# Kernel tuning notes

Measured on AMD Instinct MI355X. Metric: run time of the kernel, lower is better.

The kernel has to match this reference:

```python
import jax, jax.numpy as jnp
import numpy as np

DIM = 512
NUM_HEADS = 16
RANK = 4
HEAD_DIM = DIM // NUM_HEADS
SCALE = HEAD_DIM ** -0.5
B_, N, NW = 2048, 49, 64


def setup_inputs() -> dict:
    key = jax.random.key(0)
    ks = jax.random.split(key, 9)
    x = jax.random.normal(ks[0], (B_, N, DIM), dtype=jnp.float32)
    mask = jax.random.normal(ks[1], (NW, N, N), dtype=jnp.float32)
    # qkv base linear (torch Linear stores weight [out,in])
    W_qkv = jax.random.normal(ks[2], (3 * DIM, DIM), dtype=jnp.float32) * (DIM ** -0.5)
    b_qkv = jax.random.normal(ks[3], (3 * DIM,), dtype=jnp.float32) * 0.02
    # LoRA down [rank, dim], up [3*dim, rank] (zero-init in module; use small random for non-trivial math)
    A_down = jax.random.normal(ks[4], (RANK, DIM), dtype=jnp.float32) * 0.02
    B_up = jax.random.normal(ks[5], (3 * DIM, RANK), dtype=jnp.float32) * 0.02
    W_proj = jax.random.normal(ks[6], (DIM, DIM), dtype=jnp.float32) * (DIM ** -0.5)
    b_proj = jax.random.normal(ks[7], (DIM,), dtype=jnp.float32) * 0.02
    return {"x": x, "mask": mask, "W_qkv": W_qkv, "b_qkv": b_qkv,
            "A_down": A_down, "B_up": B_up, "W_proj": W_proj, "b_proj": b_proj}


def reference(x, mask, W_qkv, b_qkv, A_down, B_up, W_proj, b_proj):
    Bw, n, C = x.shape
    H, hd = NUM_HEADS, HEAD_DIM
    # LoRA-augmented QKV projection: base linear + up(down(x))
    qkv = x @ W_qkv.T + b_qkv + (x @ A_down.T) @ B_up.T          # [B_, N, 3C]
    qkv = qkv.reshape(Bw, n, 3, H, hd)
    q = qkv[:, :, 0].transpose(0, 2, 1, 3)                        # [B_, H, N, hd]
    k = qkv[:, :, 1].transpose(0, 2, 1, 3)
    v = qkv[:, :, 2].transpose(0, 2, 1, 3)
    attn = jnp.einsum('bhnd,bhmd->bhnm', q, k) * SCALE            # [B_, H, N, N]
    nW = mask.shape[0]
    attn = attn.reshape(Bw // nW, nW, H, n, n) + mask[None, :, None]
    attn = attn.reshape(Bw, H, n, n)
    attn = jax.nn.softmax(attn, axis=-1)
    out = jnp.einsum('bhnm,bhmd->bhnd', attn, v)                  # [B_, H, N, hd]
    out = out.transpose(0, 2, 1, 3).reshape(Bw, n, C)
    return out @ W_proj.T + b_proj
```

## Files before the change

### kernel.cpp

```cpp
#include <hip/hip_runtime.h>
#include <stdint.h>

typedef __attribute__((ext_vector_type(4))) float f32x4;
typedef __attribute__((ext_vector_type(8))) __bf16 bf16x8;
typedef __attribute__((ext_vector_type(4))) unsigned int u32x4;
typedef __attribute__((ext_vector_type(4))) unsigned short u16x4;

#define TOK 49
#define NHEAD 16
#define HDIM 32
#define CDIM 512
#define NB 2048
#define MTOT (NB * TOK)
#define ATT_SCALE 0.17677669529663687f

__device__ __forceinline__ unsigned short f2bf(float f) {
  uint32_t u = __builtin_bit_cast(uint32_t, f);
  u += 0x7FFFu + ((u >> 16) & 1u);
  return (unsigned short)(u >> 16);
}

__device__ __forceinline__ void gl_lds16(const void* g, const void* lds) {
  __builtin_amdgcn_global_load_lds(
      (__attribute__((address_space(1))) void*)(uintptr_t)g,
      (__attribute__((address_space(3))) void*)(uint32_t)(uintptr_t)lds,
      16, 0, 0);
}

__device__ __forceinline__ f32x4 mfma16(bf16x8 a, bf16x8 b, f32x4 c) {
  return __builtin_amdgcn_mfma_f32_16x16x32_bf16(a, b, c, 0, 0, 0);
}

__global__ __launch_bounds__(256) void k_prep_weff(
    const float* __restrict__ Wqkv, const float* __restrict__ Bup,
    const float* __restrict__ Adown, unsigned short* __restrict__ weff) {
  int idx = blockIdx.x * 256 + threadIdx.x;
  if (idx >= 3 * CDIM * CDIM) return;
  int o = idx >> 9, i = idx & 511;
  float v = Wqkv[idx];
#pragma unroll
  for (int r = 0; r < 4; r++) v += Bup[o * 4 + r] * Adown[r * 512 + i];
  weff[idx] = f2bf(v);
}

__global__ __launch_bounds__(256) void k_conv4(
    const float* __restrict__ src, unsigned short* __restrict__ dst, int n4) {
  for (int i = blockIdx.x * blockDim.x + threadIdx.x; i < n4;
       i += gridDim.x * blockDim.x) {
    f32x4 v = *(const f32x4*)(src + (size_t)i * 4);
    u16x4 o;
    o[0] = f2bf(v[0]); o[1] = f2bf(v[1]); o[2] = f2bf(v[2]); o[3] = f2bf(v[3]);
    *(u16x4*)(dst + (size_t)i * 4) = o;
  }
}

template <int NT, bool SPLIT>
__global__ __launch_bounds__(512, 1) void k_gemm256(
    const unsigned short* __restrict__ A, const unsigned short* __restrict__ Bw,
    const float* __restrict__ bias,
    unsigned short* __restrict__ qo, unsigned short* __restrict__ ko,
    unsigned short* __restrict__ vo, float* __restrict__ fo) {
  __shared__ __attribute__((aligned(16))) unsigned short smem[65536];
  const int t = threadIdx.x;
  const int l = t & 63;
  const int l15 = l & 15, lq = l >> 4;
  const int w = t >> 6;
  const int wr = w >> 2, wc = w & 3;
  const int bid = blockIdx.x;
  const int lb = (bid & 7) * ((int)gridDim.x >> 3) + (bid >> 3);
  const int mt = lb / NT, nt = lb % NT;
  const size_t m0 = (size_t)mt * 256;
  const int n0 = nt * 256;

  auto stageA = [&](int kt, int bb) {
    unsigned short* dst = smem + bb * 16384;
#pragma unroll
    for (int q = 0; q < 4; ++q) {
      const int li = q * 512 + t;
      const int row = li >> 3, sl = li & 7;
      gl_lds16(A + (m0 + row) * CDIM + kt * 64 + ((sl ^ (row & 7)) << 3),
               &dst[li * 8]);
    }
  };
  auto stageB = [&](int kt, int bb) {
    unsigned short* dst = smem + 32768 + bb * 16384;
#pragma unroll
    for (int q = 0; q < 4; ++q) {
      const int li = q * 512 + t;
      const int row = li >> 3, sl = li & 7;
      gl_lds16(Bw + (size_t)(n0 + row) * CDIM + kt * 64 + ((sl ^ (row & 7)) << 3),
               &dst[li * 8]);
    }
  };

  f32x4 acc[8][4] = {};
  stageA(0, 0);
  stageB(0, 0);
  for (int kt = 0; kt < 8; ++kt) {
    const int cur = kt & 1;
    if (kt < 7) {
      stageA(kt + 1, cur ^ 1);
      stageB(kt + 1, cur ^ 1);
      asm volatile("s_waitcnt vmcnt(8)" ::: "memory");
    } else {
      asm volatile("s_waitcnt vmcnt(0)" ::: "memory");
    }
    __builtin_amdgcn_s_barrier();
    asm volatile("" ::: "memory");
    const unsigned short* bufA = smem + cur * 16384;
    const unsigned short* bufB = smem + 32768 + cur * 16384;

    bf16x8 bfr[4][2];
#pragma unroll
    for (int c = 0; c < 4; ++c) {
      const int r = wc * 64 + c * 16 + l15;
#pragma unroll
      for (int h = 0; h < 2; ++h)
        bfr[c][h] = __builtin_bit_cast(
            bf16x8,
            *(const u32x4*)&bufB[r * 64 + (((lq + h * 4) ^ (r & 7)) << 3)]);
    }

    auto loadA = [&](bf16x8(&dst)[2][2], int p) {
#pragma unroll
      for (int rr = 0; rr < 2; ++rr) {
        const int r = wr * 128 + (p * 2 + rr) * 16 + l15;
#pragma unroll
        for (int h = 0; h < 2; ++h)
          dst[rr][h] = __builtin_bit_cast(
              bf16x8,
              *(const u32x4*)&bufA[r * 64 + (((lq + h * 4) ^ (r & 7)) << 3)]);
      }
    };

    bf16x8 afA[2][2], afB[2][2];
    loadA(afA, 0);
#pragma unroll
    for (int p = 0; p < 4; ++p) {
      bf16x8(&cur_)[2][2] = (p & 1) ? afB : afA;
      bf16x8(&nxt_)[2][2] = (p & 1) ? afA : afB;
      if (p < 3) loadA(nxt_, p + 1);
      __builtin_amdgcn_s_setprio(1);
#pragma unroll
      for (int rr = 0; rr < 2; ++rr) {
#pragma unroll
        for (int c = 0; c < 4; ++c) {
          acc[p * 2 + rr][c] = mfma16(cur_[rr][0], bfr[c][0], acc[p * 2 + rr][c]);
          acc[p * 2 + rr][c] = mfma16(cur_[rr][1], bfr[c][1], acc[p * 2 + rr][c]);
        }
      }
      __builtin_amdgcn_s_setprio(0);
    }
    asm volatile("" ::: "memory");
    __builtin_amdgcn_s_barrier();
  }

  __syncthreads();
  if constexpr (SPLIT) {
    unsigned short* ep = smem + w * 8192;
#pragma unroll
    for (int J = 0; J < 4; ++J) {
      const int colb = n0 + wc * 64 + J * 16 + l15;
      const float bv = bias[colb];
#pragma unroll
      for (int I = 0; I < 8; ++I) {
#pragma unroll
        for (int r = 0; r < 4; ++r)
          ep[(I * 16 + lq * 4 + r) * 64 + J * 16 + l15] =
              f2bf(acc[I][J][r] + bv);
      }
    }
    __syncthreads();
#pragma unroll
    for (int rnd = 0; rnd < 16; ++rnd) {
      const int sub = rnd * 16 + (l >> 2);
      const int mloc = sub >> 1, hd2 = sub & 1;
      const int colh = n0 + wc * 64 + hd2 * 32;
      const int which = colh >> 9;
      const int hh = (colh >> 5) & 15;
      unsigned short* dst = which == 0 ? qo : (which == 1 ? ko : vo);
      const uint32_t mg = (uint32_t)(m0 + wr * 128 + mloc);
      const uint32_t bw_ = mg / 49u;
      const uint32_t nn = mg - bw_ * 49u;
      u32x4 v = *(const u32x4*)&ep[mloc * 64 + hd2 * 32 + (l & 3) * 8];
      *(u32x4*)&dst[((size_t)(bw_ * 16u + hh) * 49u + nn) * 32u + (l & 3) * 8] =
          v;
    }
  } else {
    float* ep32 = (float*)smem + w * 4096;
#pragma unroll
    for (int ch = 0; ch < 2; ++ch) {
#pragma unroll
      for (int J = 0; J < 4; ++J) {
        const int colb = n0 + wc * 64 + J * 16 + l15;
        const float bv = bias[colb];
#pragma unroll
        for (int Ii = 0; Ii < 4; ++Ii) {
#pragma unroll
          for (int r = 0; r < 4; ++r)
            ep32[(Ii * 16 + lq * 4 + r) * 64 + J * 16 + l15] =
                acc[ch * 4 + Ii][J][r] + bv;
        }
      }
      __syncthreads();
#pragma unroll
      for (int rnd = 0; rnd < 16; ++rnd) {
        const int row = rnd * 4 + (l >> 4);
        f32x4 v = *(const f32x4*)&ep32[row * 64 + (l & 15) * 4];
        const size_t mg = m0 + wr * 128 + ch * 64 + row;
        *(f32x4*)&fo[mg * CDIM + n0 + wc * 64 + (l & 15) * 4] = v;
      }
      __syncthreads();
    }
  }
}

__global__ __launch_bounds__(256) void k_attn(
    const unsigned short* __restrict__ qb, const unsigned short* __restrict__ kb,
    const unsigned short* __restrict__ vb, const float* __restrict__ mask,
    unsigned short* __restrict__ ao) {
  __shared__ __attribute__((aligned(16))) unsigned short sP[4][64 * 64];
  __shared__ __attribute__((aligned(16))) unsigned short sV[4][32 * 64];
  const int t = threadIdx.x;
  const int l = t & 63, w = t >> 6;
  const int l15 = l & 15, lq = l >> 4;
  const int pair = blockIdx.x * 4 + w;
  const int b = pair >> 4, h = pair & 15;
  const size_t base = (size_t)pair * (TOK * HDIM);
  unsigned short* P = sP[w];
  unsigned short* Vt = sV[w];

  bf16x8 qf[4], kf[4];
#pragma unroll
  for (int i = 0; i < 4; i++)
    qf[i] = __builtin_bit_cast(
        bf16x8, *(const u32x4*)(qb + base + (size_t)(i * 16 + l15) * 32 + lq * 8));
#pragma unroll
  for (int i = 0; i < 4; i++)
    kf[i] = __builtin_bit_cast(
        bf16x8, *(const u32x4*)(kb + base + (size_t)(i * 16 + l15) * 32 + lq * 8));
  u32x4 vr[4];
#pragma unroll
  for (int j = 0; j < 4; j++)
    vr[j] = *(const u32x4*)(vb + base + (size_t)l * 32 + j * 8);

  f32x4 s[4][4];
  __builtin_amdgcn_s_setprio(1);
#pragma unroll
  for (int i = 0; i < 4; i++) {
#pragma unroll
    for (int j = 0; j < 4; j++) s[i][j] = mfma16(qf[i], kf[j], (f32x4)0.0f);
  }
  __builtin_amdgcn_s_setprio(0);

  const bool vok = (l < TOK);
  const int tsl = ((l >> 3) & 7);
  const int tlo = l & 7;
#pragma unroll
  for (int j = 0; j < 4; j++) {
#pragma unroll
    for (int c = 0; c < 4; c++) {
      uint32_t u = vr[j][c];
      int d0 = j * 8 + c * 2;
      Vt[(d0 + 0) * 64 + ((tsl ^ ((d0 + 0) & 7)) << 3) + tlo] =
          vok ? (unsigned short)(u & 0xFFFFu) : (unsigned short)0;
      Vt[(d0 + 1) * 64 + ((tsl ^ ((d0 + 1) & 7)) << 3) + tlo] =
          vok ? (unsigned short)(u >> 16) : (unsigned short)0;
    }
  }

  const float* mrow = mask + (size_t)(b & 63) * (TOK * TOK);
#pragma unroll
  for (int i = 0; i < 4; i++) {
#pragma unroll
    for (int r = 0; r < 4; r++) {
      int row = i * 16 + lq * 4 + r;
#pragma unroll
      for (int j = 0; j < 4; j++) {
        int col = j * 16 + l15;
        float xv = s[i][j][r] * ATT_SCALE;
        if (col < TOK) {
          if (row < TOK) xv += mrow[row * TOK + col];
        } else {
          xv = -1e30f;
        }
        s[i][j][r] = xv;
      }
    }
  }

  float rinv[4][4];
#pragma unroll
  for (int i = 0; i < 4; i++) {
#pragma unroll
    for (int r = 0; r < 4; r++) {
      float m = fmaxf(fmaxf(s[i][0][r], s[i][1][r]), fmaxf(s[i][2][r], s[i][3][r]));
      m = fmaxf(m, __shfl_xor(m, 1));
      m = fmaxf(m, __shfl_xor(m, 2));
      m = fmaxf(m, __shfl_xor(m, 4));
      m = fmaxf(m, __shfl_xor(m, 8));
      float sum = 0.f;
      int row = i * 16 + lq * 4 + r;
#pragma unroll
      for (int j = 0; j < 4; j++) {
        float p = __expf(s[i][j][r] - m);
        sum += p;
        P[row * 64 + (((j * 2 + (l15 >> 3)) ^ (row & 7)) << 3) + (l15 & 7)] =
            f2bf(p);
      }
      sum += __shfl_xor(sum, 1);
      sum += __shfl_xor(sum, 2);
      sum += __shfl_xor(sum, 4);
      sum += __shfl_xor(sum, 8);
      rinv[i][r] = 1.0f / sum;
    }
  }

  asm volatile("s_waitcnt lgkmcnt(0)" ::: "memory");
  __builtin_amdgcn_sched_barrier(0);

  f32x4 o[4][2] = {};
#pragma unroll
  for (int ks = 0; ks < 2; ks++) {
    bf16x8 pa[4], vf[2];
#pragma unroll
    for (int i = 0; i < 4; i++)
      pa[i] = __builtin_bit_cast(
          bf16x8,
          *(const u32x4*)&P[(i * 16 + l15) * 64 + (((lq + ks * 4) ^ (l15 & 7)) << 3)]);
#pragma unroll
    for (int j = 0; j < 2; j++)
      vf[j] = __builtin_bit_cast(
          bf16x8,
          *(const u32x4*)&Vt[(j * 16 + l15) * 64 + (((lq + ks * 4) ^ (l15 & 7)) << 3)]);
    __builtin_amdgcn_s_setprio(1);
#pragma unroll
    for (int i = 0; i < 4; i++) {
#pragma unroll
      for (int j = 0; j < 2; j++) o[i][j] = mfma16(pa[i], vf[j], o[i][j]);
    }
    __builtin_amdgcn_s_setprio(0);
  }

#pragma unroll
  for (int i = 0; i < 4; i++) {
#pragma unroll
    for (int r = 0; r < 4; r++) {
      int row = i * 16 + lq * 4 + r;
      if (row < TOK) {
        float inv = rinv[i][r];
        size_t obase = ((size_t)b * TOK + row) * CDIM + h * HDIM;
#pragma unroll
        for (int j = 0; j < 2; j++)
          ao[obase + j * 16 + l15] = f2bf(o[i][j][r] * inv);
      }
    }
  }
}

extern "C" void kernel_launch(void* const* d_in, const int* in_sizes, int n_in,
                              void* d_out, int out_size, void* d_ws,
                              size_t ws_size, hipStream_t stream) {
  const float* x = (const float*)d_in[0];
  const float* mask = (const float*)d_in[1];
  const float* Wqkv = (const float*)d_in[2];
  const float* bqkv = (const float*)d_in[3];
  const float* Adown = (const float*)d_in[4];
  const float* Bup = (const float*)d_in[5];
  const float* Wproj = (const float*)d_in[6];
  const float* bproj = (const float*)d_in[7];
  float* out = (float*)d_out;
  char* ws = (char*)d_ws;

  size_t off = 0;
  auto alloc = [&](size_t bytes) {
    size_t o = off;
    off += (bytes + 255) & ~(size_t)255;
    return o;
  };
  const size_t qkv_elems = (size_t)NB * NHEAD * TOK * HDIM;
  unsigned short* weff = (unsigned short*)(ws + alloc((size_t)3 * CDIM * CDIM * 2));
  unsigned short* wpb = (unsigned short*)(ws + alloc((size_t)CDIM * CDIM * 2));
  unsigned short* qb = (unsigned short*)(ws + alloc(qkv_elems * 2 + 4096));
  unsigned short* kb = (unsigned short*)(ws + alloc(qkv_elems * 2 + 4096));
  unsigned short* vb = (unsigned short*)(ws + alloc(qkv_elems * 2 + 4096));
  unsigned short* xb = (unsigned short*)(ws + alloc((size_t)MTOT * CDIM * 2));
  unsigned short* ao = xb;

  k_prep_weff<<<(3 * CDIM * CDIM + 255) / 256, 256, 0, stream>>>(Wqkv, Bup,
                                                                 Adown, weff);
  k_conv4<<<256, 256, 0, stream>>>(Wproj, wpb, CDIM * CDIM / 4);
  k_conv4<<<2048, 256, 0, stream>>>(x, xb, MTOT * CDIM / 4);
  k_gemm256<6, true><<<(MTOT / 256) * 6, 512, 0, stream>>>(
      xb, weff, bqkv, qb, kb, vb, nullptr);
  k_attn<<<NB * NHEAD / 4, 256, 0, stream>>>(qb, kb, vb, mask, ao);
  k_gemm256<2, false><<<(MTOT / 256) * 2, 512, 0, stream>>>(
      ao, wpb, bproj, nullptr, nullptr, nullptr, out);
}
```

Before: 559.4 us.

## Fuse fp32-to-bf16 input conversion into QKV GEMM A-tile staging and swizzle epilogue LDS

The QKV GEMM now reads x directly as fp32 through registers, converts to bf16, and writes into the swizzled LDS tile. Writes for the next k-tile are interleaved between MFMA phases, which removes the separate conversion kernel and its bf16 round-trip through global memory. Separately, the A-fragment double buffering across p phases is removed, and both epilogues use XOR-swizzled LDS addressing to reduce bank conflicts. In exchange, the QKV GEMM reads twice as many A bytes, which are recomputed 6 times across N tiles, and it adds register pressure plus VALU conversion work inside the main loop.

```diff
diff --git a/kernel.cpp b/kernel.cpp
--- a/kernel.cpp
+++ b/kernel.cpp
@@ -54,13 +54,15 @@
   }
 }
 
-template <int NT, bool SPLIT>
+template <int NT, bool SPLIT, bool AF32>
 __global__ __launch_bounds__(512, 1) void k_gemm256(
-    const unsigned short* __restrict__ A, const unsigned short* __restrict__ Bw,
+    const void* __restrict__ Ain, const unsigned short* __restrict__ Bw,
     const float* __restrict__ bias,
     unsigned short* __restrict__ qo, unsigned short* __restrict__ ko,
     unsigned short* __restrict__ vo, float* __restrict__ fo) {
   __shared__ __attribute__((aligned(16))) unsigned short smem[65536];
+  const unsigned short* Ab = (const unsigned short*)Ain;
+  const float* Af = (const float*)Ain;
   const int t = threadIdx.x;
   const int l = t & 63;
   const int l15 = l & 15, lq = l >> 4;
@@ -78,7 +80,7 @@
     for (int q = 0; q < 4; ++q) {
       const int li = q * 512 + t;
       const int row = li >> 3, sl = li & 7;
-      gl_lds16(A + (m0 + row) * CDIM + kt * 64 + ((sl ^ (row & 7)) << 3),
+      gl_lds16(Ab + (m0 + row) * CDIM + kt * 64 + ((sl ^ (row & 7)) << 3),
                &dst[li * 8]);
     }
   };
@@ -93,14 +95,53 @@
     }
   };
 
+  f32x4 ar[4];
+  auto issueAh = [&](int kt, int h) {
+#pragma unroll
+    for (int q = 0; q < 2; ++q) {
+      const int li = (h * 2 + q) * 512 + t;
+      const int row = li >> 3, sl = li & 7;
+      const float* p =
+          Af + (m0 + row) * CDIM + kt * 64 + ((sl ^ (row & 7)) << 3);
+      ar[q * 2] = *(const f32x4*)p;
+      ar[q * 2 + 1] = *(const f32x4*)(p + 4);
+    }
+  };
+  auto writeAh = [&](int bb, int h) {
+    unsigned short* dst = smem + bb * 16384;
+#pragma unroll
+    for (int q = 0; q < 2; ++q) {
+      const int li = (h * 2 + q) * 512 + t;
+      u32x4 wv;
+      wv[0] = (uint32_t)f2bf(ar[q * 2][0]) | ((uint32_t)f2bf(ar[q * 2][1]) << 16);
+      wv[1] = (uint32_t)f2bf(ar[q * 2][2]) | ((uint32_t)f2bf(ar[q * 2][3]) << 16);
+      wv[2] = (uint32_t)f2bf(ar[q * 2 + 1][0]) |
+              ((uint32_t)f2bf(ar[q * 2 + 1][1]) << 16);
+      wv[3] = (uint32_t)f2bf(ar[q * 2 + 1][2]) |
+              ((uint32_t)f2bf(ar[q * 2 + 1][3]) << 16);
+      *(u32x4*)&dst[li * 8] = wv;
+    }
+  };
+
   f32x4 acc[8][4] = {};
-  stageA(0, 0);
-  stageB(0, 0);
+  if constexpr (AF32) {
+    issueAh(0, 0);
+    stageB(0, 0);
+    writeAh(0, 0);
+    issueAh(0, 1);
+    writeAh(0, 1);
+    asm volatile("s_waitcnt lgkmcnt(0)" ::: "memory");
+  } else {
+    stageA(0, 0);
+    stageB(0, 0);
+  }
+
   for (int kt = 0; kt < 8; ++kt) {
-    const int cur = kt & 1;
+    const int cur = kt & 1, nb = cur ^ 1;
     if (kt < 7) {
-      stageA(kt + 1, cur ^ 1);
-      stageB(kt + 1, cur ^ 1);
+      if constexpr (AF32) issueAh(kt + 1, 0);
+      else stageA(kt + 1, nb);
+      stageB(kt + 1, nb);
       asm volatile("s_waitcnt vmcnt(8)" ::: "memory");
     } else {
       asm volatile("s_waitcnt vmcnt(0)" ::: "memory");
@@ -121,36 +162,38 @@
             *(const u32x4*)&bufB[r * 64 + (((lq + h * 4) ^ (r & 7)) << 3)]);
     }
 
-    auto loadA = [&](bf16x8(&dst)[2][2], int p) {
+#pragma unroll
+    for (int p = 0; p < 4; ++p) {
+      bf16x8 af[2][2];
 #pragma unroll
       for (int rr = 0; rr < 2; ++rr) {
         const int r = wr * 128 + (p * 2 + rr) * 16 + l15;
 #pragma unroll
         for (int h = 0; h < 2; ++h)
-          dst[rr][h] = __builtin_bit_cast(
+          af[rr][h] = __builtin_bit_cast(
               bf16x8,
               *(const u32x4*)&bufA[r * 64 + (((lq + h * 4) ^ (r & 7)) << 3)]);
       }
-    };
-
-    bf16x8 afA[2][2], afB[2][2];
-    loadA(afA, 0);
-#pragma unroll
-    for (int p = 0; p < 4; ++p) {
-      bf16x8(&cur_)[2][2] = (p & 1) ? afB : afA;
-      bf16x8(&nxt_)[2][2] = (p & 1) ? afA : afB;
-      if (p < 3) loadA(nxt_, p + 1);
       __builtin_amdgcn_s_setprio(1);
 #pragma unroll
       for (int rr = 0; rr < 2; ++rr) {
 #pragma unroll
         for (int c = 0; c < 4; ++c) {
-          acc[p * 2 + rr][c] = mfma16(cur_[rr][0], bfr[c][0], acc[p * 2 + rr][c]);
-          acc[p * 2 + rr][c] = mfma16(cur_[rr][1], bfr[c][1], acc[p * 2 + rr][c]);
+          acc[p * 2 + rr][c] = mfma16(af[rr][0], bfr[c][0], acc[p * 2 + rr][c]);
+          acc[p * 2 + rr][c] = mfma16(af[rr][1], bfr[c][1], acc[p * 2 + rr][c]);
         }
       }
       __builtin_amdgcn_s_setprio(0);
-    }
+      if constexpr (AF32) {
+        if (p == 1 && kt < 7) {
+          writeAh(nb, 0);
+          issueAh(kt + 1, 1);
+        }
+        if (p == 3 && kt < 7) writeAh(nb, 1);
+      }
+    }
+    if constexpr (AF32)
+      asm volatile("s_waitcnt lgkmcnt(0)" ::: "memory");
     asm volatile("" ::: "memory");
     __builtin_amdgcn_s_barrier();
   }
@@ -162,12 +205,15 @@
     for (int J = 0; J < 4; ++J) {
       const int colb = n0 + wc * 64 + J * 16 + l15;
       const float bv = bias[colb];
+      const int sl0 = J * 2 + (l15 >> 3);
 #pragma unroll
       for (int I = 0; I < 8; ++I) {
 #pragma unroll
-        for (int r = 0; r < 4; ++r)
-          ep[(I * 16 + lq * 4 + r) * 64 + J * 16 + l15] =
+        for (int r = 0; r < 4; ++r) {
+          const int row = I * 16 + lq * 4 + r;
+          ep[row * 64 + ((sl0 ^ (row & 7)) << 3) + (l15 & 7)] =
               f2bf(acc[I][J][r] + bv);
+        }
       }
     }
     __syncthreads();
@@ -182,7 +228,8 @@
       const uint32_t mg = (uint32_t)(m0 + wr * 128 + mloc);
       const uint32_t bw_ = mg / 49u;
       const uint32_t nn = mg - bw_ * 49u;
-      u32x4 v = *(const u32x4*)&ep[mloc * 64 + hd2 * 32 + (l & 3) * 8];
+      const int sl = hd2 * 4 + (l & 3);
+      u32x4 v = *(const u32x4*)&ep[mloc * 64 + ((sl ^ (mloc & 7)) << 3)];
       *(u32x4*)&dst[((size_t)(bw_ * 16u + hh) * 49u + nn) * 32u + (l & 3) * 8] =
           v;
     }
@@ -194,19 +241,23 @@
       for (int J = 0; J < 4; ++J) {
         const int colb = n0 + wc * 64 + J * 16 + l15;
         const float bv = bias[colb];
+        const int sl0 = J * 4 + (l15 >> 2);
 #pragma unroll
         for (int Ii = 0; Ii < 4; ++Ii) {
 #pragma unroll
-          for (int r = 0; r < 4; ++r)
-            ep32[(Ii * 16 + lq * 4 + r) * 64 + J * 16 + l15] =
+          for (int r = 0; r < 4; ++r) {
+            const int row = Ii * 16 + lq * 4 + r;
+            ep32[row * 64 + ((sl0 ^ (row & 7)) << 2) + (l15 & 3)] =
                 acc[ch * 4 + Ii][J][r] + bv;
+          }
         }
       }
       __syncthreads();
 #pragma unroll
       for (int rnd = 0; rnd < 16; ++rnd) {
         const int row = rnd * 4 + (l >> 4);
-        f32x4 v = *(const f32x4*)&ep32[row * 64 + (l & 15) * 4];
+        const int sl = l & 15;
+        f32x4 v = *(const f32x4*)&ep32[row * 64 + ((sl ^ (row & 7)) << 2)];
         const size_t mg = m0 + wr * 128 + ch * 64 + row;
         *(f32x4*)&fo[mg * CDIM + n0 + wc * 64 + (l & 15) * 4] = v;
       }
@@ -384,16 +435,14 @@
   unsigned short* qb = (unsigned short*)(ws + alloc(qkv_elems * 2 + 4096));
   unsigned short* kb = (unsigned short*)(ws + alloc(qkv_elems * 2 + 4096));
   unsigned short* vb = (unsigned short*)(ws + alloc(qkv_elems * 2 + 4096));
-  unsigned short* xb = (unsigned short*)(ws + alloc((size_t)MTOT * CDIM * 2));
-  unsigned short* ao = xb;
+  unsigned short* ao = (unsigned short*)(ws + alloc((size_t)MTOT * CDIM * 2));
 
   k_prep_weff<<<(3 * CDIM * CDIM + 255) / 256, 256, 0, stream>>>(Wqkv, Bup,
                                                                  Adown, weff);
   k_conv4<<<256, 256, 0, stream>>>(Wproj, wpb, CDIM * CDIM / 4);
-  k_conv4<<<2048, 256, 0, stream>>>(x, xb, MTOT * CDIM / 4);
-  k_gemm256<6, true><<<(MTOT / 256) * 6, 512, 0, stream>>>(
-      xb, weff, bqkv, qb, kb, vb, nullptr);
+  k_gemm256<6, true, true><<<(MTOT / 256) * 6, 512, 0, stream>>>(
+      x, weff, bqkv, qb, kb, vb, nullptr);
   k_attn<<<NB * NHEAD / 4, 256, 0, stream>>>(qb, kb, vb, mask, ao);
-  k_gemm256<2, false><<<(MTOT / 256) * 2, 512, 0, stream>>>(
+  k_gemm256<2, false, false><<<(MTOT / 256) * 2, 512, 0, stream>>>(
       ao, wpb, bproj, nullptr, nullptr, nullptr, out);
 }
```

Result: slower. 583.4 us (+4.3%).
